# Optimization experiments

Hardware: AMD Instinct MI355X
Metric: run time of the kernel (lower is better)

## Reference

```python
import jax, jax.numpy as jnp
import numpy as np

ALPHA = 0.8   # blend between colored and original content feature
EPS = 1e-6    # added to content eigenvalues before inverse sqrt
K_C = 8       # number of content clusters (segmentation labels)
K_S = 8       # number of style clusters (HDBSCAN labels)


def setup_inputs() -> dict:
    key = jax.random.key(0)
    k0, k1, k2, k3, k4 = jax.random.split(key, 5)
    b, c, wh, swh = 1, 512, 16384, 16384  # VGG relu4_1 of a 1024x1024 image
    return {
        "cf": jax.random.normal(k0, (b, c, wh), dtype=jnp.float32),
        "sf": jax.random.normal(k1, (b, c, swh), dtype=jnp.float32),
        "match_scores": jax.random.uniform(k2, (K_C, K_S), dtype=jnp.float32, minval=0.1, maxval=1.0),
        "cl_labels": jax.random.randint(k3, (wh,), 0, K_C, dtype=jnp.int64),
        "sl_labels": jax.random.randint(k4, (swh,), 0, K_S, dtype=jnp.int64),
    }


def _wct_one_cluster(cf, m, scores, s_sums, s_S2, s_counts):
    # cf [b,c,wh]; m [wh] 0/1 mask of this content cluster; scores [Ks]
    # s_sums [Ks,b,c] = sum of sf over each style cluster
    # s_S2   [Ks,b,c,c] = sum of sf sf^T over each style cluster
    n = m.sum()
    # --- content whitening ---
    c_mean = jnp.einsum('bcp,p->bc', cf, m) / n                       # [b,c]
    centered = (cf - c_mean[:, :, None]) * m                          # [b,c,wh]
    c_cov = jnp.einsum('bcp,bdp->bcd', centered, centered) / (n - 1.0)
    c_u, c_e, c_vh = jnp.linalg.svd(c_cov, full_matrices=False)
    c_v = jnp.swapaxes(c_vh, -1, -2)
    c_d = (c_e + EPS) ** -0.5                                         # [b,c]
    W = (c_v * c_d[:, None, :]) @ jnp.swapaxes(c_u, -1, -2)           # c_v diag(d) c_u^T
    whitened = W @ centered                                           # [b,c,wh]
    # --- weighted style statistics (closed form over style clusters) ---
    total = jnp.sum(scores * s_counts)                                # weighted pixel count
    s_mean = jnp.einsum('k,kbc->bc', scores, s_sums) / total          # [b,c]
    s_cov = (jnp.einsum('k,kbcd->bcd', scores, s_S2)
             - total * jnp.einsum('bc,bd->bcd', s_mean, s_mean)) / (total - 1.0)
    s_u, s_e, s_vh = jnp.linalg.svd(s_cov, full_matrices=False)
    C = (s_u * jnp.sqrt(s_e)[:, None, :]) @ s_vh                      # s_u diag(sqrt(e)) s_v^T
    colored = C @ whitened + s_mean[:, :, None]                       # [b,c,wh]
    return ALPHA * colored + (1.0 - ALPHA) * cf


def reference(cf, sf, match_scores, cl_labels, sl_labels):
    # cf [b,c,wh], sf [b,c,swh], match_scores [Kc,Ks], labels int per pixel
    c_masks = (cl_labels[None, :] == jnp.arange(K_C)[:, None]).astype(cf.dtype)  # [Kc,wh]
    s_masks = (sl_labels[None, :] == jnp.arange(K_S)[:, None]).astype(sf.dtype)  # [Ks,swh]
    s_counts = s_masks.sum(axis=1)                                    # [Ks]
    s_sums = jnp.einsum('bcp,kp->kbc', sf, s_masks)                   # [Ks,b,c]
    s_S2 = jnp.einsum('kp,bcp,bdp->kbcd', s_masks, sf, sf)            # [Ks,b,c,c]
    outs = jax.vmap(lambda m, sc: _wct_one_cluster(cf, m, sc, s_sums, s_S2, s_counts))(
        c_masks, match_scores)                                        # [Kc,b,c,wh]
    # scatter back: each pixel takes the output of its own content cluster
    cs_feature = jnp.einsum('kp,kbcp->bcp', c_masks, outs)
    return cs_feature
```

## Files before the change

kernel.cpp:

```cpp
#include <hip/hip_runtime.h>
#include <math.h>

#define C_DIM 512
#define WH    16384
#define CAP   17408
#define NBX   136
#define SEG_ALIGN 128
#define NCHUNK 64
#define CHUNK  256
#define NMAT 16
#define NSLICE 4
#define MSZ  (C_DIM*C_DIM)
#define ALPHA_C 0.8f
#define EPS_C   1e-6f
#define NIT 5

typedef __attribute__((ext_vector_type(8))) __bf16 bfrag;
typedef __attribute__((ext_vector_type(4))) float f32x4;

__device__ inline float bf2f(ushort h){ return __uint_as_float(((unsigned)h)<<16); }
__device__ inline void split2(float v, ushort& h, ushort& l){
    unsigned u = __float_as_uint(v);
    h = (ushort)(u >> 16);
    float r = v - __uint_as_float(u & 0xffff0000u);
    l = (ushort)(__float_as_uint(r) >> 16);
}

__device__ __forceinline__ int xcd_swz(int bid, int nwg){
    int c = nwg >> 3;
    return (bid & 7)*c + (bid >> 3);
}

__device__ __forceinline__ void gload16(const void* g, void* l){
    __builtin_amdgcn_global_load_lds(
        (const __attribute__((address_space(1))) unsigned int*)g,
        (__attribute__((address_space(3))) unsigned int*)l, 16, 0, 0);
}

template<int R>
__device__ __forceinline__ void stage_panelR(const ushort* __restrict__ src,
        int stride, int i0, int k0, ushort* lds){
    int t = threadIdx.x;
    #pragma unroll
    for (int i = 0; i < R/32; ++i){
        int slot = t + i*256;
        int row = slot >> 3, c8 = slot & 7;
        const ushort* g = src + (size_t)(i0+row)*stride + k0 + ((c8 ^ (row&7))<<3);
        gload16((const void*)g, (void*)&lds[(size_t)(i*256 + (t & 192))*8]);
    }
}

template<int MFR>
__device__ __forceinline__ void mfma_block(const ushort* As0, const ushort* As1,
        const ushort* Bs0, const ushort* Bs1, f32x4 (&acc)[MFR][4],
        int wm, int wn, int lr, int lk){
    #pragma unroll
    for (int kk = 0; kk < 64; kk += 32){
        bfrag ah[MFR], al[MFR], bh[4], bl[4];
        #pragma unroll
        for (int m = 0; m < MFR; ++m){
            int row = wm*(MFR*16) + m*16 + lr;
            int off = (row*64 + kk + lk*8) ^ ((row&7)<<3);
            ah[m] = *(const bfrag*)&As0[off];
            al[m] = *(const bfrag*)&As1[off];
        }
        #pragma unroll
        for (int n = 0; n < 4; ++n){
            int row = wn*64 + n*16 + lr;
            int off = (row*64 + kk + lk*8) ^ ((row&7)<<3);
            bh[n] = *(const bfrag*)&Bs0[off];
            bl[n] = *(const bfrag*)&Bs1[off];
        }
        #pragma unroll
        for (int m = 0; m < MFR; ++m)
            #pragma unroll
            for (int n = 0; n < 4; ++n){
                acc[m][n] = __builtin_amdgcn_mfma_f32_16x16x32_bf16(ah[m], bh[n], acc[m][n], 0,0,0);
                acc[m][n] = __builtin_amdgcn_mfma_f32_16x16x32_bf16(ah[m], bl[n], acc[m][n], 0,0,0);
                acc[m][n] = __builtin_amdgcn_mfma_f32_16x16x32_bf16(al[m], bh[n], acc[m][n], 0,0,0);
            }
    }
}

template<int MFR>
__device__ __forceinline__ void mm_coreT(const ushort* __restrict__ Am, size_t aPl, int aStr,
        const ushort* __restrict__ Bm, size_t bPl, int bStr,
        int i0, int j0, int kLo, int kHi,
        ushort (&As)[2][MFR*2048], ushort (&Bs)[2][8192], f32x4 (&acc)[MFR][4],
        int wm, int wn, int lr, int lk){
    for (int k0 = kLo; k0 < kHi; k0 += 64){
        stage_panelR<MFR*32>(Am,       aStr, i0, k0, As[0]);
        stage_panelR<MFR*32>(Am + aPl, aStr, i0, k0, As[1]);
        stage_panelR<128>(Bm,       bStr, j0, k0, Bs[0]);
        stage_panelR<128>(Bm + bPl, bStr, j0, k0, Bs[1]);
        __syncthreads();
        mfma_block<MFR>(As[0], As[1], Bs[0], Bs[1], acc, wm, wn, lr, lk);
        __syncthreads();
    }
}


__global__ __launch_bounds__(256) void k_chunk_hist(const int* __restrict__ lab0,
        const int* __restrict__ lab1, int* __restrict__ ch0, int* __restrict__ ch1){
    __shared__ int h[8];
    int t = threadIdx.x;
    const int* labels = blockIdx.y ? lab1 : lab0;
    int* chunkCnt = blockIdx.y ? ch1 : ch0;
    if (t < 8) h[t] = 0;
    __syncthreads();
    int l = labels[blockIdx.x*CHUNK + t];
    atomicAdd(&h[l], 1);
    __syncthreads();
    if (t < 8) chunkCnt[blockIdx.x*8 + t] = h[t];
}

__global__ void k_scan(const int* __restrict__ ch0, const int* __restrict__ ch1,
                       int* __restrict__ cnt0, int* __restrict__ cnt1,
                       int* __restrict__ off0, int* __restrict__ off1,
                       int* __restrict__ base0, int* __restrict__ base1){
    int which = threadIdx.x;
    if (which >= 2) return;
    const int* chunkCnt = which ? ch1 : ch0;
    int* cnt = which ? cnt1 : cnt0;
    int* offPad = which ? off1 : off0;
    int* base = which ? base1 : base0;
    int c[8];
    for (int k=0;k<8;k++) c[k]=0;
    for (int ch=0; ch<NCHUNK; ch++)
        for (int k=0;k<8;k++) c[k] += chunkCnt[ch*8+k];
    int off = 0;
    for (int k=0;k<8;k++){
        cnt[k] = c[k];
        offPad[k] = off;
        off += ((c[k] + SEG_ALIGN - 1)/SEG_ALIGN)*SEG_ALIGN;
    }
    offPad[8] = off;
    for (int k=0;k<8;k++){
        int run = offPad[k];
        for (int ch=0; ch<NCHUNK; ch++){
            base[ch*8+k] = run;
            run += chunkCnt[ch*8+k];
        }
    }
}

__global__ void k_place(const int* __restrict__ lab0, const int* __restrict__ lab1,
        const int* __restrict__ base0, const int* __restrict__ base1,
        int* __restrict__ perm0, int* __restrict__ perm1, int* __restrict__ inv0){
    int t = threadIdx.x;
    if (t >= 8) return;
    const int* labels = blockIdx.y ? lab1 : lab0;
    const int* base = blockIdx.y ? base1 : base0;
    int* perm = blockIdx.y ? perm1 : perm0;
    int* inv = blockIdx.y ? nullptr : inv0;
    int ch = blockIdx.x;
    int pos = base[ch*8+t];
    int s = ch*CHUNK;
    for (int i=0;i<CHUNK;i++){
        if (labels[s+i] == t){
            perm[pos] = s+i;
            if (inv) inv[s+i] = pos;
            pos++;
        }
    }
}


__global__ __launch_bounds__(256) void k_gather2(const float* __restrict__ src0,
        const float* __restrict__ src1,
        const int* __restrict__ perm0, const int* __restrict__ perm1,
        const int* __restrict__ off0, const int* __restrict__ off1,
        const int* __restrict__ cnt0, const int* __restrict__ cnt1,
        ushort* __restrict__ dH0, ushort* __restrict__ dL0,
        ushort* __restrict__ dH1, ushort* __restrict__ dL1,
        float* __restrict__ ps0, float* __restrict__ ps1,
        int* __restrict__ sg0, int* __restrict__ sg1){
    int z = blockIdx.z;
    const float* src = z ? src1 : src0;
    const int* perm = z ? perm1 : perm0;
    const int* offPad = z ? off1 : off0;
    const int* cnt = z ? cnt1 : cnt0;
    ushort* dstH = z ? dH1 : dH0;
    ushort* dstL = z ? dL1 : dL0;
    float* psum = z ? ps1 : ps0;
    int* segOf = z ? sg1 : sg0;
    __shared__ int so[9], sc[8];
    __shared__ int pcache[128];
    int t = threadIdx.x;
    if (t < 9) so[t] = offPad[t];
    if (t < 8) sc[t] = cnt[t];
    __syncthreads();
    int bx = blockIdx.x;
    int i0 = bx*128;
    if (t < 128) pcache[t] = (i0 + t < so[8]) ? perm[i0 + t] : 0;
    __syncthreads();
    int k = 0;
    while (k < 7 && i0 >= so[k+1]) k++;
    int n = sc[k], s0 = so[k];
    int ch = t >> 4, px0 = (t & 15)*8;
    int c  = blockIdx.y*16 + ch;
    const float* row = src + (size_t)c*WH;
    float v[8];
    #pragma unroll
    for (int x=0;x<8;x++){
        int i = i0 + px0 + x;
        v[x] = (i - s0 < n) ? row[pcache[px0+x]] : 0.0f;
    }
    float s = 0.0f;
    ushort hv[8], lv[8];
    #pragma unroll
    for (int x=0;x<8;x++){
        s += v[x];
        split2(v[x], hv[x], lv[x]);
    }
    *(uint4*)&dstH[(size_t)c*CAP + i0 + px0] = *(uint4*)hv;
    *(uint4*)&dstL[(size_t)c*CAP + i0 + px0] = *(uint4*)lv;
    #pragma unroll
    for (int d=1; d<16; d<<=1) s += __shfl_xor(s, d, 16);
    if ((t & 15) == 0) psum[(size_t)c*NBX + bx] = s;
    if (t == 0) segOf[bx] = k;
}


__global__ __launch_bounds__(256) void k_meanred(const float* __restrict__ ps0,
        const float* __restrict__ ps1, const int* __restrict__ sg0,
        const int* __restrict__ sg1, const int* __restrict__ cnt0,
        float* __restrict__ out0, float* __restrict__ out1){
    int z = blockIdx.z;
    const float* psum = z ? ps1 : ps0;
    const int* segOf = z ? sg1 : sg0;
    float* out = z ? out1 : out0;
    int k = blockIdx.x;
    int c = blockIdx.y*256 + threadIdx.x;
    float s = 0.0f;
    for (int bx=0; bx<NBX; bx++)
        if (segOf[bx] == k) s += psum[(size_t)c*NBX + bx];
    out[k*C_DIM + c] = z ? s : s/(float)cnt0[k];
}


__global__ __launch_bounds__(256) void k_transpose(const ushort* __restrict__ S,
                                                   ushort* __restrict__ D){
    __shared__ ushort tile[64][72];
    int p = blockIdx.z;
    const ushort* Sp = S + (size_t)p*C_DIM*CAP;
    ushort* Dp = D + (size_t)p*CAP*C_DIM;
    int cb = blockIdx.x*64;
    int rb = blockIdx.y*64;
    int t = threadIdx.x;
    int tr = t >> 3, tc = t & 7;
    #pragma unroll
    for (int i=0;i<2;i++){
        int r = tr + i*32;
        uint4 v = *(const uint4*)&Sp[(size_t)(rb+r)*CAP + cb + tc*8];
        ushort* u = (ushort*)&v;
        #pragma unroll
        for (int j=0;j<8;j++) tile[tc*8+j][r] = u[j];
    }
    __syncthreads();
    #pragma unroll
    for (int i=0;i<2;i++){
        int r = tr + i*32;
        uint4 v;
        ushort* u = (ushort*)&v;
        #pragma unroll
        for (int j=0;j<8;j++) u[j] = tile[r][tc*8+j];
        *(uint4*)&Dp[(size_t)(cb+r)*C_DIM + rb + tc*8] = v;
    }
}

__global__ __launch_bounds__(256) void k_style_mean(const float* __restrict__ scores,
        const int* __restrict__ cntS, const float* __restrict__ ssum,
        float* __restrict__ total, float* __restrict__ smean){
    int t = threadIdx.x;
    __shared__ float tot[8];
    if (t < 8){
        float s = 0.0f;
        for (int j=0;j<8;j++) s += scores[t*8+j]*(float)cntS[j];
        tot[t] = s; total[t] = s;
    }
    __syncthreads();
    for (int idx=t; idx<8*C_DIM; idx+=256){
        int k = idx / C_DIM, c = idx % C_DIM;
        float s = 0.0f;
        for (int j=0;j<8;j++) s += scores[k*8+j]*ssum[j*C_DIM+c];
        smean[idx] = s / tot[k];
    }
}


__global__ __launch_bounds__(256,2) void k_syrk_mfma(
        const ushort* __restrict__ Xc, const ushort* __restrict__ Xs,
        const int* __restrict__ offC, const int* __restrict__ offS,
        float* __restrict__ Pf){
    __shared__ ushort As[2][8192];
    __shared__ ushort Bs[2][8192];
    int wg = xcd_swz(blockIdx.x, NMAT*NSLICE*10);
    int mat = wg / (NSLICE*10);
    int rem = wg % (NSLICE*10);
    int slice = rem / 10, tt = rem % 10;
    int ti, tj;
    if (tt < 4){ ti=0; tj=tt; }
    else if (tt < 7){ ti=1; tj=tt-3; }
    else if (tt < 9){ ti=2; tj=tt-5; }
    else { ti=3; tj=3; }
    const ushort* X = (mat < 8) ? Xc : Xs;
    const int* offP = (mat < 8) ? offC : offS;
    int cl = mat & 7;
    int off = offP[cl], npad = offP[cl+1] - off;
    int i0 = ti*128, j0 = tj*128;
    int L = ((npad + NSLICE*64 - 1)/(NSLICE*64))*64;
    int k_lo = slice*L;
    int k_hi = min(k_lo + L, npad);
    int t = threadIdx.x;
    int lane = t & 63, wave = t >> 6;
    int wm = wave >> 1, wn = wave & 1;
    int lr = lane & 15, lk = lane >> 4;
    f32x4 zero = {0.f,0.f,0.f,0.f};
    f32x4 acc[4][4];
    #pragma unroll
    for (int m=0;m<4;m++)
        #pragma unroll
        for (int n=0;n<4;n++) acc[m][n] = zero;
    mm_coreT<4>(X + off, (size_t)C_DIM*CAP, CAP,
                X + off, (size_t)C_DIM*CAP, CAP,
                i0, j0, k_lo, k_hi, As, Bs, acc, wm, wn, lr, lk);
    float* O = Pf + ((size_t)(slice*16 + mat))*MSZ;
    #pragma unroll
    for (int m=0;m<4;m++)
        #pragma unroll
        for (int n=0;n<4;n++)
            #pragma unroll
            for (int j=0;j<4;j++){
                int gr = i0 + wm*64 + m*16 + lk*4 + j;
                int gc = j0 + wn*64 + n*16 + lr;
                O[(size_t)gr*C_DIM + gc] = acc[m][n][j];
            }
}


__global__ __launch_bounds__(256) void k_assemble(const float* __restrict__ P0,
        const float* __restrict__ scores, const float* __restrict__ total,
        const float* __restrict__ cmean, const float* __restrict__ smean,
        const int* __restrict__ cntC, ushort* __restrict__ bA){
    const size_t S = (size_t)NMAT*MSZ;
    __shared__ ushort tH[64][136];
    __shared__ ushort tL[64][136];
    int mat = blockIdx.y;
    int tt = blockIdx.x;
    int ti, tj;
    if (tt < 4){ ti=0; tj=tt; }
    else if (tt < 7){ ti=1; tj=tt-3; }
    else if (tt < 9){ ti=2; tj=tt-5; }
    else { ti=3; tj=3; }
    int i0 = ti*128, j0 = tj*128;
    int t = threadIdx.x;
    ushort* bm = bA + (size_t)mat*2*MSZ;
    int k = mat - 8;
    float nOrTot = (mat < 8) ? (float)cntC[mat] : total[k];
    float inv_nm1 = 1.0f/(nOrTot - 1.0f);
    const float* mrow = (mat < 8) ? (cmean + mat*C_DIM) : (smean + k*C_DIM);
    for (int h = 0; h < 2; ++h){
        #pragma unroll
        for (int rep = 0; rep < 4; ++rep){
            int lin = rep*2048 + t*8;
            int r = lin >> 7;
            int c = lin & 127;
            int gr = i0 + h*64 + r;
            int gc = j0 + c;
            size_t e = (size_t)gr*C_DIM + gc;
            float s2[8];
            if (mat < 8){
                size_t b = (size_t)mat*MSZ + e;
                #pragma unroll
                for (int x=0;x<8;x++)
                    s2[x] = P0[b+x] + P0[b+S+x] + P0[b+2*S+x] + P0[b+3*S+x];
            } else {
                #pragma unroll
                for (int x=0;x<8;x++) s2[x] = 0.0f;
                #pragma unroll
                for (int jj=0;jj<8;jj++){
                    float sc = scores[k*8+jj];
                    size_t b = (size_t)(8+jj)*MSZ + e;
                    #pragma unroll
                    for (int x=0;x<8;x++)
                        s2[x] += sc*(P0[b+x] + P0[b+S+x] + P0[b+2*S+x] + P0[b+3*S+x]);
                }
            }
            float mi = mrow[gr];
            #pragma unroll
            for (int x=0;x<8;x++){
                float v = (s2[x] - nOrTot*mi*mrow[gc+x])*inv_nm1;
                if (mat < 8 && gr == gc+x) v += EPS_C;
                ushort hh,ll; split2(v,hh,ll);
                bm[e+x] = hh; bm[MSZ+e+x] = ll;
                tH[r][c+x] = hh; tL[r][c+x] = ll;
            }
        }
        if (ti != tj){
            __syncthreads();
            #pragma unroll
            for (int rep = 0; rep < 4; ++rep){
                int lin = rep*2048 + t*8;
                int rr = lin >> 6;
                int cc0 = lin & 63;
                size_t eo = (size_t)(j0+rr)*C_DIM + i0 + h*64 + cc0;
                #pragma unroll
                for (int x=0;x<8;x++){
                    bm[eo+x]     = tH[cc0+x][rr];
                    bm[MSZ+eo+x] = tL[cc0+x][rr];
                }
            }
            __syncthreads();
        }
    }
}


__global__ __launch_bounds__(256) void k_mm_rowsum(
        const ushort* __restrict__ A, float* __restrict__ rowpart){
    __shared__ ushort As[2][4096];
    __shared__ ushort Bs[2][8192];
    __shared__ float rs[64][2];
    int wg = xcd_swz(blockIdx.x, NMAT*32);
    int mat = wg >> 5, tile = wg & 31;
    int ti = tile >> 2, tj = tile & 3;
    int i0 = ti*64, j0 = tj*128;
    const ushort* Am = A + (size_t)mat*2*MSZ;
    int t = threadIdx.x;
    int lane = t & 63, wave = t >> 6;
    int wm = wave >> 1, wn = wave & 1;
    int lr = lane & 15, lk = lane >> 4;
    f32x4 zero = {0.f,0.f,0.f,0.f};
    f32x4 acc[2][4];
    #pragma unroll
    for (int m=0;m<2;m++)
        #pragma unroll
        for (int n=0;n<4;n++) acc[m][n] = zero;
    mm_coreT<2>(Am, MSZ, C_DIM, Am, MSZ, C_DIM, i0, j0, 0, C_DIM,
                As, Bs, acc, wm, wn, lr, lk);
    #pragma unroll
    for (int m=0;m<2;m++)
        #pragma unroll
        for (int j=0;j<4;j++){
            float s = 0.0f;
            #pragma unroll
            for (int n=0;n<4;n++) s += fabsf(acc[m][n][j]);
            #pragma unroll
            for (int d=1; d<16; d<<=1) s += __shfl_xor(s, d);
            if (lr == 0) rs[wm*32 + m*16 + lk*4 + j][wn] = s;
        }
    __syncthreads();
    if (t < 64)
        rowpart[((size_t)mat*4 + tj)*512 + i0 + t] = rs[t][0] + rs[t][1];
}


__global__ __launch_bounds__(256) void k_tmax(const float* __restrict__ rowpart,
                                              float* __restrict__ tvals){
    int mat = blockIdx.x, t = threadIdx.x;
    const float* rp = rowpart + (size_t)mat*4*512;
    float mx = 0.0f;
    for (int r = t; r < 512; r += 256){
        float s = rp[r] + rp[512+r] + rp[1024+r] + rp[1536+r];
        mx = fmaxf(mx, s);
    }
    __shared__ float red[256];
    red[t] = mx; __syncthreads();
    for (int s=128; s>0; s>>=1){ if (t<s) red[t]=fmaxf(red[t],red[t+s]); __syncthreads(); }
    if (t == 0) tvals[mat] = 0.5f*sqrtf(red[0]);
}


__global__ __launch_bounds__(256) void k_initP0(const ushort* __restrict__ bA,
        const float* __restrict__ tvals, ushort* __restrict__ P){
    int mat = blockIdx.y;
    int e = blockIdx.x*256 + threadIdx.x;
    size_t base = (size_t)mat*2*MSZ;
    float inv = 1.0f / tvals[mat];
    float a = (bf2f(bA[base+e]) + bf2f(bA[base+MSZ+e])) * inv;
    int i = e >> 9, j = e & 511;
    float p = ((i==j)?1.5f:0.0f) - 0.5f*a;
    ushort h,l; split2(p,h,l);
    P[base + e] = h;
    P[base + MSZ + e] = l;
}


template<int EPI>
__global__ __launch_bounds__(256) void k_mm_ns64(
        const ushort* __restrict__ A, const ushort* __restrict__ B,
        ushort* __restrict__ Co, float* __restrict__ Cf,
        const float* __restrict__ tvals, int nmat){
    __shared__ ushort As[2][4096];
    __shared__ ushort Bs[2][8192];
    int wg = xcd_swz(blockIdx.x, nmat*32);
    int mat = wg >> 5, tile = wg & 31;
    int i0 = (tile>>2)*64, j0 = (tile&3)*128;
    const ushort* Am = A + (size_t)mat*2*MSZ;
    const ushort* Bm = B + (size_t)mat*2*MSZ;
    int t = threadIdx.x;
    int lane = t & 63, wave = t >> 6;
    int wm = wave >> 1, wn = wave & 1;
    int lr = lane & 15, lk = lane >> 4;
    f32x4 zero = {0.f,0.f,0.f,0.f};
    f32x4 acc[2][4];
    #pragma unroll
    for (int m=0;m<2;m++)
        #pragma unroll
        for (int n=0;n<4;n++) acc[m][n] = zero;
    mm_coreT<2>(Am, MSZ, C_DIM, Bm, MSZ, C_DIM, i0, j0, 0, C_DIM,
                As, Bs, acc, wm, wn, lr, lk);
    if (EPI == 3){
        float* Cm = Cf + (size_t)mat*MSZ;
        ushort* Mh = Co + (size_t)mat*2*MSZ;
        ushort* Ml = Mh + MSZ;
        float ascale = ALPHA_C * sqrtf(tvals[8+mat]/tvals[mat]);
        #pragma unroll
        for (int m=0;m<2;m++)
            #pragma unroll
            for (int n=0;n<4;n++)
                #pragma unroll
                for (int j=0;j<4;j++){
                    int gr = i0 + wm*32 + m*16 + lk*4 + j;
                    int gc = j0 + wn*64 + n*16 + lr;
                    float v = acc[m][n][j];
                    size_t idx = (size_t)gr*C_DIM + gc;
                    Cm[idx] = v;
                    float mv = ascale*v + ((gr==gc)?(1.0f-ALPHA_C):0.0f);
                    ushort h,l; split2(mv,h,l);
                    Mh[idx] = h; Ml[idx] = l;
                }
    } else {
        float sc = (EPI == 4) ? 1.0f/tvals[mat] : 1.0f;
        ushort* Ch = Co + (size_t)mat*2*MSZ;
        ushort* Cl = Ch + MSZ;
        #pragma unroll
        for (int m=0;m<2;m++)
            #pragma unroll
            for (int n=0;n<4;n++)
                #pragma unroll
                for (int j=0;j<4;j++){
                    int gr = i0 + wm*32 + m*16 + lk*4 + j;
                    int gc = j0 + wn*64 + n*16 + lr;
                    float v = acc[m][n][j];
                    if (EPI == 1) v = ((gr==gc)?1.5f:0.0f) - 0.5f*v;
                    if (EPI == 4) v *= sc;
                    ushort h,l; split2(v,h,l);
                    size_t idx = (size_t)gr*C_DIM + gc;
                    Ch[idx] = h;
                    Cl[idx] = l;
                }
    }
}


__global__ __launch_bounds__(256,2) void k_mm_ns2(
        const ushort* __restrict__ Y, const ushort* __restrict__ P,
        const ushort* __restrict__ Z, ushort* __restrict__ fy,
        ushort* __restrict__ fz){
    __shared__ ushort As[2][8192];
    __shared__ ushort Bs[2][8192];
    int wg = xcd_swz(blockIdx.x, NMAT*32);
    int mat = wg >> 5;
    int r = wg & 31;
    int op = r >> 4, tile = r & 15;
    int i0 = (tile>>2)*128, j0 = (tile&3)*128;
    const ushort* Am = (op ? P : Y) + (size_t)mat*2*MSZ;
    const ushort* Bm = (op ? Z : P) + (size_t)mat*2*MSZ;
    ushort* Ch = (op ? fz : fy) + (size_t)mat*2*MSZ;
    ushort* Cl = Ch + MSZ;
    int t = threadIdx.x;
    int lane = t & 63, wave = t >> 6;
    int wm = wave >> 1, wn = wave & 1;
    int lr = lane & 15, lk = lane >> 4;
    f32x4 zero = {0.f,0.f,0.f,0.f};
    f32x4 acc[4][4];
    #pragma unroll
    for (int m=0;m<4;m++)
        #pragma unroll
        for (int n=0;n<4;n++) acc[m][n] = zero;
    mm_coreT<4>(Am, MSZ, C_DIM, Bm, MSZ, C_DIM, i0, j0, 0, C_DIM,
                As, Bs, acc, wm, wn, lr, lk);
    #pragma unroll
    for (int m=0;m<4;m++)
        #pragma unroll
        for (int n=0;n<4;n++)
            #pragma unroll
            for (int j=0;j<4;j++){
                int gr = i0 + wm*64 + m*16 + lk*4 + j;
                int gc = j0 + wn*64 + n*16 + lr;
                ushort h,l; split2(acc[m][n][j],h,l);
                size_t idx = (size_t)gr*C_DIM + gc;
                Ch[idx] = h;
                Cl[idx] = l;
            }
}


__global__ __launch_bounds__(256) void k_mm_ns2_last(
        const ushort* __restrict__ Y, const ushort* __restrict__ P,
        const ushort* __restrict__ Z, ushort* __restrict__ fy,
        ushort* __restrict__ fz){
    __shared__ ushort As[2][4096];
    __shared__ ushort Bs[2][8192];
    int wg = xcd_swz(blockIdx.x, NMAT*32);
    int mat = wg >> 5, tile = wg & 31;
    int op = (mat < 8) ? 1 : 0;
    int i0 = (tile>>2)*64, j0 = (tile&3)*128;
    const ushort* Am = (op ? P : Y) + (size_t)mat*2*MSZ;
    const ushort* Bm = (op ? Z : P) + (size_t)mat*2*MSZ;
    ushort* Ch = (op ? fz : fy) + (size_t)mat*2*MSZ;
    ushort* Cl = Ch + MSZ;
    int t = threadIdx.x;
    int lane = t & 63, wave = t >> 6;
    int wm = wave >> 1, wn = wave & 1;
    int lr = lane & 15, lk = lane >> 4;
    f32x4 zero = {0.f,0.f,0.f,0.f};
    f32x4 acc[2][4];
    #pragma unroll
    for (int m=0;m<2;m++)
        #pragma unroll
        for (int n=0;n<4;n++) acc[m][n] = zero;
    mm_coreT<2>(Am, MSZ, C_DIM, Bm, MSZ, C_DIM, i0, j0, 0, C_DIM,
                As, Bs, acc, wm, wn, lr, lk);
    #pragma unroll
    for (int m=0;m<2;m++)
        #pragma unroll
        for (int n=0;n<4;n++)
            #pragma unroll
            for (int j=0;j<4;j++){
                int gr = i0 + wm*32 + m*16 + lk*4 + j;
                int gc = j0 + wn*64 + n*16 + lr;
                ushort h,l; split2(acc[m][n][j],h,l);
                size_t idx = (size_t)gr*C_DIM + gc;
                Ch[idx] = h;
                Cl[idx] = l;
            }
}


__global__ __launch_bounds__(256) void k_buildV(const float* __restrict__ T,
        const float* __restrict__ tvals, const float* __restrict__ cmean,
        const float* __restrict__ smean, float* __restrict__ vvec){
    __shared__ float cm[512];
    int k = blockIdx.x, t = threadIdx.x;
    cm[t] = cmean[k*C_DIM + t];
    cm[t+256] = cmean[k*C_DIM + t + 256];
    __syncthreads();
    float scale = ALPHA_C * sqrtf(tvals[8+k]/tvals[k]);
    int c = blockIdx.y*256 + t;
    const float* row = T + (size_t)k*MSZ + (size_t)c*C_DIM;
    float s = 0.0f;
    for (int d=0; d<C_DIM; d++) s = fmaf(row[d], cm[d], s);
    vvec[k*C_DIM + c] = ALPHA_C*smean[k*C_DIM + c] - scale*s;
}


__global__ __launch_bounds__(256,2) void k_apply_mfma(
        const ushort* __restrict__ Msp, const ushort* __restrict__ XT,
        const float* __restrict__ vvec, const int* __restrict__ offPad,
        float* __restrict__ Sg){
    __shared__ ushort As[2][8192];
    __shared__ ushort Bs[2][8192];
    __shared__ int so[9];
    int t = threadIdx.x;
    if (t < 9) so[t] = offPad[t];
    __syncthreads();
    int wg = xcd_swz(blockIdx.x, (CAP/128)*4);
    int j0 = (wg>>2)*128;
    int i0 = (wg&3)*128;
    if (j0 >= so[8]) return;
    int cl = 0;
    while (cl < 7 && j0 >= so[cl+1]) cl++;
    const ushort* Am = Msp + (size_t)cl*2*MSZ;
    int lane = t & 63, wave = t >> 6;
    int wm = wave >> 1, wn = wave & 1;
    int lr = lane & 15, lk = lane >> 4;
    f32x4 zero = {0.f,0.f,0.f,0.f};
    f32x4 acc[4][4];
    #pragma unroll
    for (int m=0;m<4;m++)
        #pragma unroll
        for (int n=0;n<4;n++) acc[m][n] = zero;
    mm_coreT<4>(Am, MSZ, C_DIM, XT, (size_t)CAP*C_DIM, C_DIM, i0, j0, 0, C_DIM,
                As, Bs, acc, wm, wn, lr, lk);
    #pragma unroll
    for (int m=0;m<4;m++)
        #pragma unroll
        for (int nn=0;nn<4;nn++)
            #pragma unroll
            for (int j=0;j<4;j++){
                int gr = i0 + wm*64 + m*16 + lk*4 + j;
                int gc = j0 + wn*64 + nn*16 + lr;
                Sg[(size_t)gr*CAP + gc] = acc[m][nn][j] + vvec[cl*C_DIM + gr];
            }
}


__global__ __launch_bounds__(256) void k_scatter(const float* __restrict__ Sg,
        const int* __restrict__ ginv, float* __restrict__ out){
    size_t idx = (size_t)blockIdx.x*256 + threadIdx.x;
    int p = (int)(idx & (WH-1));
    int c = (int)(idx >> 14);
    out[idx] = Sg[(size_t)c*CAP + ginv[p]];
}


extern "C" void kernel_launch(void* const* d_in, const int* in_sizes, int n_in,
                              void* d_out, int out_size, void* d_ws, size_t ws_size,
                              hipStream_t stream) {
    (void)in_sizes; (void)n_in;
    const float* cf     = (const float*)d_in[0];
    const float* sf     = (const float*)d_in[1];
    const float* scores = (const float*)d_in[2];
    const int*   cl     = (const int*)d_in[3];
    const int*   sl     = (const int*)d_in[4];
    float* out = (float*)d_out;
    float* ws  = (float*)d_ws;

    size_t o = 0;
    ushort* XcH = (ushort*)(ws + o);
    float*  Sg  = ws + o;       o += (size_t)C_DIM*CAP;
    ushort* XcL = XcH + (size_t)C_DIM*CAP;
    ushort* XsH = (ushort*)(ws + o); o += (size_t)C_DIM*CAP;
    float* S4  = ws + o; o += (size_t)NMAT*MSZ;
    float* NS0 = ws + o; o += (size_t)4*NMAT*MSZ;
    float* cmean = ws + o; o += 8*C_DIM;
    float* ssum  = ws + o; o += 8*C_DIM;
    float* smean = ws + o; o += 8*C_DIM;
    float* vvec  = ws + o; o += 8*C_DIM;
    float* tvals = ws + o; o += 16;
    float* rowpart = ws + o; o += (size_t)NMAT*4*512;
    float* total = ws + o; o += 8;
    float* psumC = ws + o; o += (size_t)C_DIM*NBX;
    float* psumS = ws + o; o += (size_t)C_DIM*NBX;
    int* ip = (int*)(ws + o);
    int* permC    = ip; ip += CAP;
    int* permCinv = ip; ip += CAP;
    int* permS    = ip; ip += CAP;
    int* segOfC = ip; ip += NBX;
    int* segOfS = ip; ip += NBX;
    int* cntC  = ip; ip += 8;
    int* cntS  = ip; ip += 8;
    int* offC  = ip; ip += 9;
    int* offS  = ip; ip += 9;
    int* chC   = ip; ip += NCHUNK*8;
    int* chS   = ip; ip += NCHUNK*8;
    int* baseC = ip; ip += NCHUNK*8;
    int* baseS = ip; ip += NCHUNK*8;
    size_t need_bytes = (size_t)((char*)ip - (char*)d_ws);
    if (ws_size < need_bytes){
        hipMemcpyAsync(d_out, (const void*)cf, (size_t)out_size*sizeof(float),
                       hipMemcpyDeviceToDevice, stream);
        return;
    }
    float* Pf = NS0;
    ushort* s0 = (ushort*)(NS0 + 0*(size_t)NMAT*MSZ);
    ushort* s1 = (ushort*)(NS0 + 1*(size_t)NMAT*MSZ);
    ushort* s2 = (ushort*)(NS0 + 2*(size_t)NMAT*MSZ);
    ushort* s3 = (ushort*)(NS0 + 3*(size_t)NMAT*MSZ);
    ushort* s4 = (ushort*)S4;

    k_chunk_hist<<<dim3(NCHUNK,2),256,0,stream>>>(cl, sl, chC, chS);
    k_scan<<<1,64,0,stream>>>(chC, chS, cntC, cntS, offC, offS, baseC, baseS);
    k_place<<<dim3(NCHUNK,2),64,0,stream>>>(cl, sl, baseC, baseS, permC, permS, permCinv);

    dim3 gg(NBX, C_DIM/16, 2);
    k_gather2<<<gg,256,0,stream>>>(cf, sf, permC, permS, offC, offS, cntC, cntS,
                                   XcH, XcL, XsH, XsH + (size_t)C_DIM*CAP,
                                   psumC, psumS, segOfC, segOfS);

    k_meanred<<<dim3(8,2,2),256,0,stream>>>(psumC, psumS, segOfC, segOfS, cntC,
                                            cmean, ssum);
    k_style_mean<<<1,256,0,stream>>>(scores, cntS, ssum, total, smean);

    k_syrk_mfma<<<NMAT*NSLICE*10,256,0,stream>>>(XcH, XsH, offC, offS, Pf);

    k_transpose<<<dim3(CAP/64, C_DIM/64, 2),256,0,stream>>>(XcH, XsH);
    ushort* XT = XsH;

    ushort* bA = s4;
    k_assemble<<<dim3(10,16),256,0,stream>>>(Pf, scores, total, cmean, smean, cntC, bA);

    k_mm_rowsum<<<NMAT*32,256,0,stream>>>(bA, rowpart);
    k_tmax<<<NMAT,256,0,stream>>>(rowpart, tvals);

    k_initP0<<<dim3(MSZ/256,NMAT),256,0,stream>>>(bA, tvals, s1);
    k_mm_ns64<4><<<NMAT*32,256,0,stream>>>(bA, s1, s2, nullptr, tvals, NMAT);

    ushort* bY = s2;  ushort* bZ = s1;  ushort* bP = s3;
    ushort* fy = s4;  ushort* fz = s0;
    for (int it=0; it<NIT-1; ++it){
        k_mm_ns64<1><<<NMAT*32,256,0,stream>>>(bZ, bY, bP, nullptr, nullptr, NMAT);
        if (it < NIT-2)
            k_mm_ns2<<<NMAT*32,256,0,stream>>>(bY, bP, bZ, fy, fz);
        else
            k_mm_ns2_last<<<NMAT*32,256,0,stream>>>(bY, bP, bZ, fy, fz);
        ushort* t1;
        t1 = bY; bY = fy; fy = t1;
        t1 = bZ; bZ = fz; fz = t1;
    }
    float* Tf = (float*)fy;
    ushort* Msp = fz;
    k_mm_ns64<3><<<8*32,256,0,stream>>>(bY + (size_t)8*2*MSZ, bZ, Msp, Tf, tvals, 8);

    k_buildV<<<dim3(8,2),256,0,stream>>>(Tf, tvals, cmean, smean, vvec);

    k_apply_mfma<<<(CAP/128)*4,256,0,stream>>>(Msp, XT, vvec, offC, Sg);
    k_scatter<<<(C_DIM*WH)/256,256,0,stream>>>(Sg, permCinv, out);
}
```

Before: 520.3 us.

## Exploit symmetry in Newton-Schulz products by computing upper-triangle tiles and mirroring

Measured after the change: 520.2 us. About the same (-0.0%).

```diff
diff --git a/kernel.cpp b/kernel.cpp
--- a/kernel.cpp
+++ b/kernel.cpp
@@ -555,17 +555,25 @@
 }
 
 
-__global__ __launch_bounds__(256,2) void k_mm_ns2(
+__global__ __launch_bounds__(256) void k_mm_ns2(
         const ushort* __restrict__ Y, const ushort* __restrict__ P,
         const ushort* __restrict__ Z, ushort* __restrict__ fy,
         ushort* __restrict__ fz){
-    __shared__ ushort As[2][8192];
-    __shared__ ushort Bs[2][8192];
-    int wg = xcd_swz(blockIdx.x, NMAT*32);
-    int mat = wg >> 5;
-    int r = wg & 31;
-    int op = r >> 4, tile = r & 15;
-    int i0 = (tile>>2)*128, j0 = (tile&3)*128;
+    __shared__ ushort lds[24576];
+    ushort* As0 = lds;
+    ushort* As1 = lds + 4096;
+    ushort* Bs0 = lds + 8192;
+    ushort* Bs1 = lds + 16384;
+    int wg = xcd_swz(blockIdx.x, NMAT*40);
+    int mat = wg / 40;
+    int rem = wg % 40;
+    int op = rem / 20, tt = rem % 20;
+    int ti, tj;
+    if (tt < 2){ tj=0; ti=tt; }
+    else if (tt < 6){ tj=1; ti=tt-2; }
+    else if (tt < 12){ tj=2; ti=tt-6; }
+    else { tj=3; ti=tt-12; }
+    int i0 = ti*64, j0 = tj*128;
     const ushort* Am = (op ? P : Y) + (size_t)mat*2*MSZ;
     const ushort* Bm = (op ? Z : P) + (size_t)mat*2*MSZ;
     ushort* Ch = (op ? fz : fy) + (size_t)mat*2*MSZ;
@@ -575,26 +583,50 @@
     int wm = wave >> 1, wn = wave & 1;
     int lr = lane & 15, lk = lane >> 4;
     f32x4 zero = {0.f,0.f,0.f,0.f};
-    f32x4 acc[4][4];
-    #pragma unroll
-    for (int m=0;m<4;m++)
+    f32x4 acc[2][4];
+    #pragma unroll
+    for (int m=0;m<2;m++)
         #pragma unroll
         for (int n=0;n<4;n++) acc[m][n] = zero;
-    mm_coreT<4>(Am, MSZ, C_DIM, Bm, MSZ, C_DIM, i0, j0, 0, C_DIM,
-                As, Bs, acc, wm, wn, lr, lk);
-    #pragma unroll
-    for (int m=0;m<4;m++)
+    for (int k0 = 0; k0 < C_DIM; k0 += 64){
+        stage_panelR<64>(Am,        C_DIM, i0, k0, As0);
+        stage_panelR<64>(Am + MSZ,  C_DIM, i0, k0, As1);
+        stage_panelR<128>(Bm,       C_DIM, j0, k0, Bs0);
+        stage_panelR<128>(Bm + MSZ, C_DIM, j0, k0, Bs1);
+        __syncthreads();
+        mfma_block<2>(As0, As1, Bs0, Bs1, acc, wm, wn, lr, lk);
+        __syncthreads();
+    }
+    bool strict_up = (ti < 2*tj);
+    ushort* stgH = lds;
+    ushort* stgL = lds + 8704;
+    #pragma unroll
+    for (int m=0;m<2;m++)
         #pragma unroll
         for (int n=0;n<4;n++)
             #pragma unroll
             for (int j=0;j<4;j++){
-                int gr = i0 + wm*64 + m*16 + lk*4 + j;
-                int gc = j0 + wn*64 + n*16 + lr;
+                int rl = wm*32 + m*16 + lk*4 + j;
+                int cll = wn*64 + n*16 + lr;
+                int gr = i0 + rl, gc = j0 + cll;
                 ushort h,l; split2(acc[m][n][j],h,l);
                 size_t idx = (size_t)gr*C_DIM + gc;
                 Ch[idx] = h;
                 Cl[idx] = l;
+                if (strict_up){
+                    stgH[cll*68 + rl] = h;
+                    stgL[cll*68 + rl] = l;
+                }
             }
+    if (strict_up){
+        __syncthreads();
+        int r = t >> 1, pl = t & 1;
+        const ushort* src = (pl ? stgL : stgH) + r*68;
+        ushort* dst = (pl ? Cl : Ch) + (size_t)(j0 + r)*C_DIM + i0;
+        #pragma unroll
+        for (int x=0;x<16;x++)
+            ((uint2*)dst)[x] = ((const uint2*)src)[x];
+    }
 }
 
 
@@ -794,7 +826,7 @@
     for (int it=0; it<NIT-1; ++it){
         k_mm_ns64<1><<<NMAT*32,256,0,stream>>>(bZ, bY, bP, nullptr, nullptr, NMAT);
         if (it < NIT-2)
-            k_mm_ns2<<<NMAT*32,256,0,stream>>>(bY, bP, bZ, fy, fz);
+            k_mm_ns2<<<NMAT*40,256,0,stream>>>(bY, bP, bZ, fy, fz);
         else
             k_mm_ns2_last<<<NMAT*32,256,0,stream>>>(bY, bP, bZ, fy, fz);
         ushort* t1;
```
